# Optimization experiments

Hardware: AMD Instinct MI355X
Metric: run time of the kernel (lower is better)

The kernel has to match this reference:

```python
import jax, jax.numpy as jnp
import numpy as np

N = 10000      # nodes
E = 160000     # directed edges (avg degree 16)
F_IN = 2208    # num_features (DenseNet-161 dim)
H = 512        # hidden_channels
C = 2          # num_classes


def setup_inputs() -> dict:
    key = jax.random.key(0)
    ks = jax.random.split(key, 10)
    x = jax.random.normal(ks[0], (N, F_IN), dtype=jnp.float32)
    edge_index = jax.random.randint(ks[1], (2, E), 0, N, dtype=jnp.int64)
    batch = jnp.zeros((N,), dtype=jnp.int64)

    def glorot(k, fan_in, fan_out):
        s = np.sqrt(6.0 / (fan_in + fan_out)).astype(np.float32)
        return jax.random.uniform(k, (fan_in, fan_out), jnp.float32, -s, s)

    return {
        "x": x,
        "edge_index": edge_index,
        "batch": batch,
        "W1": glorot(ks[2], F_IN, H), "b1": jnp.zeros((H,), jnp.float32),
        "W2": glorot(ks[3], H, H),    "b2": jnp.zeros((H,), jnp.float32),
        "W3": glorot(ks[4], H, H),    "b3": jnp.zeros((H,), jnp.float32),
        "W4": glorot(ks[5], H, C),    "b4": jnp.zeros((C,), jnp.float32),
    }


def reference(x, edge_index, batch, W1, b1, W2, b2, W3, b3, W4, b4):
    # GCNConv (PyG defaults): add self-loops, symmetric normalization
    # out = D^{-1/2} (A + I) D^{-1/2} X W + b. Norm depends only on the
    # graph, so compute it once and reuse across the 4 layers.
    src, dst = edge_index[0], edge_index[1]
    loop = jnp.arange(N, dtype=edge_index.dtype)
    s = jnp.concatenate([src, loop])  # [E+N]
    d = jnp.concatenate([dst, loop])  # [E+N]
    deg = jax.ops.segment_sum(jnp.ones(E + N, x.dtype), d, num_segments=N)
    dinv = jnp.where(deg > 0, jax.lax.rsqrt(deg), 0.0)
    norm = dinv[s] * dinv[d]          # [E+N] per-edge weight

    def conv(h, W, b):
        h = h @ W                                 # [N, out] dense GEMM first (PyG order)
        msg = h[s] * norm[:, None]                # gather + scale  [E+N, out]
        return jax.ops.segment_sum(msg, d, num_segments=N) + b

    h = jax.nn.relu(conv(x, W1, b1))   # dropout p=0.3 is identity in eval mode
    h = jax.nn.relu(conv(h, W2, b2))
    h = jax.nn.relu(conv(h, W3, b3))
    h = conv(h, W4, b4)
    return jax.nn.log_softmax(h, axis=1)
```

## Files before the change

### kernel.cpp

```cpp
#include <hip/hip_runtime.h>
#include <hip/hip_bf16.h>

#define NNODES 10000
#define NEDGES 160000
#define FIN    2208
#define HDIM   512
#define NCLS   2

#define MPAD   10240
#define K1PAD  2240

typedef __bf16 bf16x8 __attribute__((ext_vector_type(8)));
typedef float  f32x4  __attribute__((ext_vector_type(4)));
typedef unsigned short u16x8 __attribute__((ext_vector_type(8)));

__device__ inline unsigned short f2bf(float f) {
    union { float f; unsigned int u; } v; v.f = f;
    return (unsigned short)((v.u + 0x7FFFu + ((v.u >> 16) & 1u)) >> 16);
}
__device__ inline float bf2f(unsigned short u) {
    union { unsigned int i; float f; } v; v.i = ((unsigned int)u) << 16; return v.f;
}


__global__ void k_init(int* cnt, int* row_cnt, int n) {
    int i = blockIdx.x * blockDim.x + threadIdx.x;
    if (i < n) { cnt[i] = 0; row_cnt[i] = 0; }
}

__global__ void k_hist(const int* __restrict__ ei, int* __restrict__ cnt, int e) {
    int i = blockIdx.x * blockDim.x + threadIdx.x;
    if (i < e) atomicAdd(&cnt[ei[NEDGES + i]], 1);
}

__global__ void k_scan(const int* __restrict__ cnt, int* __restrict__ row_ptr, int n) {
    __shared__ int wsum[16];
    __shared__ int s_carry;
    int tid = threadIdx.x;
    int lane = tid & 63, wid = tid >> 6;
    if (tid == 0) { s_carry = 0; row_ptr[0] = 0; }
    __syncthreads();
    for (int base = 0; base < n; base += 1024) {
        int i = base + tid;
        int v = (i < n) ? cnt[i] : 0;
        #pragma unroll
        for (int off = 1; off < 64; off <<= 1) {
            int t = __shfl_up(v, off);
            if (lane >= off) v += t;
        }
        if (lane == 63) wsum[wid] = v;
        __syncthreads();
        if (wid == 0) {
            int s = (lane < 16) ? wsum[lane] : 0;
            #pragma unroll
            for (int off = 1; off < 16; off <<= 1) {
                int t = __shfl_up(s, off);
                if (lane >= off) s += t;
            }
            if (lane < 16) wsum[lane] = s;
        }
        __syncthreads();
        int add = s_carry + ((wid > 0) ? wsum[wid - 1] : 0);
        if (i < n) row_ptr[i + 1] = v + add;
        __syncthreads();
        if (tid == 1023) s_carry += wsum[15];
        __syncthreads();
    }
}

__global__ void k_dinv(const int* __restrict__ cnt, float* __restrict__ dinv, int n) {
    int i = blockIdx.x * blockDim.x + threadIdx.x;
    if (i < n) dinv[i] = rsqrtf((float)cnt[i] + 1.0f);
}

__global__ void k_fill(const int* __restrict__ ei, const int* __restrict__ row_ptr,
                       int* __restrict__ row_cnt, int* __restrict__ col_src, int e) {
    int i = blockIdx.x * blockDim.x + threadIdx.x;
    if (i < e) {
        int src = ei[i];
        int dst = ei[NEDGES + i];
        int pos = row_ptr[dst] + atomicAdd(&row_cnt[dst], 1);
        col_src[pos] = src;
    }
}


__global__ void k_cvt_x(const float* __restrict__ x, unsigned short* __restrict__ xb) {
    int row = blockIdx.x;
    int t = threadIdx.x;
    unsigned short* orow = xb + (size_t)row * K1PAD;
    u16x8 z = {0, 0, 0, 0, 0, 0, 0, 0};
    if (row >= NNODES) {
        for (int c = t; c < K1PAD / 8; c += 256) *(u16x8*)(orow + c * 8) = z;
        return;
    }
    const float* irow = x + (size_t)row * FIN;
    for (int c = t; c < K1PAD / 8; c += 256) {
        int col = c * 8;
        u16x8 o = z;
        if (col + 8 <= FIN) {
            float4 f0 = *(const float4*)(irow + col);
            float4 f1 = *(const float4*)(irow + col + 4);
            o[0] = f2bf(f0.x); o[1] = f2bf(f0.y); o[2] = f2bf(f0.z); o[3] = f2bf(f0.w);
            o[4] = f2bf(f1.x); o[5] = f2bf(f1.y); o[6] = f2bf(f1.z); o[7] = f2bf(f1.w);
        }
        *(u16x8*)(orow + col) = o;
    }
}

__global__ void k_cvt_wt(const float* __restrict__ W, unsigned short* __restrict__ Wt,
                         int Kreal, int Kp) {
    int k = blockIdx.x * 256 + threadIdx.x;
    int n = blockIdx.y;
    if (k >= Kp) return;
    float v = (k < Kreal) ? W[(size_t)k * HDIM + n] : 0.0f;
    Wt[(size_t)n * Kp + k] = f2bf(v);
}


#define BKK 64

__global__ __launch_bounds__(256) void k_gemm_bf16(
    const unsigned short* __restrict__ A,
    const unsigned short* __restrict__ Bt,
    unsigned short* __restrict__ C,
    int M, int K) {
    __shared__ char As[128 * BKK * 2] __attribute__((aligned(16)));
    __shared__ char Bs[128 * BKK * 2] __attribute__((aligned(16)));
    const int tid  = threadIdx.x;
    const int lane = tid & 63;
    const int w    = tid >> 6;
    const int wm   = w & 1, wn = w >> 1;
    const int quad = lane >> 4, lq = lane & 15;

    const int l    = blockIdx.x;
    const int xcd  = l & 7;
    const int j    = l >> 3;
    const int bm   = ((j >> 2) * 8 + xcd) * 128;
    const int bn   = (j & 3) * 128;

    f32x4 acc[4][4] = {};

    for (int k0 = 0; k0 < K; k0 += BKK) {
        #pragma unroll
        for (int i = 0; i < 4; ++i) {
            int c  = i * 256 + tid;
            int r  = c >> 3;
            int g  = (c & 7) ^ (r & 7);
            const char* gpA = (const char*)A  + ((size_t)(bm + r) * K + k0) * 2 + (g << 4);
            const char* gpB = (const char*)Bt + ((size_t)(bn + r) * K + k0) * 2 + (g << 4);
            __builtin_amdgcn_global_load_lds(
                (const __attribute__((address_space(1))) void*)gpA,
                (__attribute__((address_space(3))) void*)(As + c * 16), 16, 0, 0);
            __builtin_amdgcn_global_load_lds(
                (const __attribute__((address_space(1))) void*)gpB,
                (__attribute__((address_space(3))) void*)(Bs + c * 16), 16, 0, 0);
        }
        __syncthreads();

        #pragma unroll
        for (int s = 0; s < 2; ++s) {
            bf16x8 af[4], bfr[4];
            #pragma unroll
            for (int i = 0; i < 4; ++i) {
                int r = wm * 64 + i * 16 + lq;
                int g = s * 4 + quad;
                af[i]  = *(const bf16x8*)(As + r * 128 + ((g ^ (r & 7)) << 4));
                int n = wn * 64 + i * 16 + lq;
                bfr[i] = *(const bf16x8*)(Bs + n * 128 + ((g ^ (n & 7)) << 4));
            }
            #pragma unroll
            for (int i = 0; i < 4; ++i)
                #pragma unroll
                for (int jj = 0; jj < 4; ++jj)
                    acc[i][jj] = __builtin_amdgcn_mfma_f32_16x16x32_bf16(
                        af[i], bfr[jj], acc[i][jj], 0, 0, 0);
        }
        __syncthreads();
    }

    #pragma unroll
    for (int i = 0; i < 4; ++i) {
        #pragma unroll
        for (int p = 0; p < 4; ++p) {
            int r = bm + wm * 64 + i * 16 + quad * 4 + p;
            if (r < M) {
                #pragma unroll
                for (int jj = 0; jj < 4; ++jj) {
                    int col = bn + wn * 64 + jj * 16 + lq;
                    C[(size_t)r * HDIM + col] = f2bf(acc[i][jj][p]);
                }
            }
        }
    }
}


__global__ void k_agg(const unsigned short* __restrict__ Y, const float* __restrict__ dinv,
                      const int* __restrict__ row_ptr, const int* __restrict__ col_src,
                      const float* __restrict__ bias, unsigned short* __restrict__ Hb,
                      int do_relu) {
    int w = (blockIdx.x * blockDim.x + threadIdx.x) >> 6;
    int lane = threadIdx.x & 63;
    if (w >= MPAD) return;
    unsigned short* hr = Hb + (size_t)w * HDIM + lane * 8;
    if (w >= NNODES) {
        u16x8 z = {0, 0, 0, 0, 0, 0, 0, 0};
        *(u16x8*)hr = z;
        return;
    }
    float di = dinv[w];
    float sw = di * di;
    u16x8 own = *(const u16x8*)(Y + (size_t)w * HDIM + lane * 8);
    float acc[8];
    #pragma unroll
    for (int t = 0; t < 8; ++t) acc[t] = sw * bf2f(own[t]);

    int e0 = row_ptr[w], e1 = row_ptr[w + 1];
    int e = e0;
    for (; e + 4 <= e1; e += 4) {
        int s0 = col_src[e + 0], s1 = col_src[e + 1];
        int s2 = col_src[e + 2], s3 = col_src[e + 3];
        float w0 = di * dinv[s0], w1 = di * dinv[s1];
        float w2 = di * dinv[s2], w3 = di * dinv[s3];
        u16x8 v0 = *(const u16x8*)(Y + (size_t)s0 * HDIM + lane * 8);
        u16x8 v1 = *(const u16x8*)(Y + (size_t)s1 * HDIM + lane * 8);
        u16x8 v2 = *(const u16x8*)(Y + (size_t)s2 * HDIM + lane * 8);
        u16x8 v3 = *(const u16x8*)(Y + (size_t)s3 * HDIM + lane * 8);
        #pragma unroll
        for (int t = 0; t < 8; ++t) {
            acc[t] += w0 * bf2f(v0[t]);
            acc[t] += w1 * bf2f(v1[t]);
            acc[t] += w2 * bf2f(v2[t]);
            acc[t] += w3 * bf2f(v3[t]);
        }
    }
    for (; e < e1; ++e) {
        int s = col_src[e];
        float wg = di * dinv[s];
        u16x8 v = *(const u16x8*)(Y + (size_t)s * HDIM + lane * 8);
        #pragma unroll
        for (int t = 0; t < 8; ++t) acc[t] += wg * bf2f(v[t]);
    }

    float4 b0 = ((const float4*)bias)[lane * 2];
    float4 b1 = ((const float4*)bias)[lane * 2 + 1];
    acc[0] += b0.x; acc[1] += b0.y; acc[2] += b0.z; acc[3] += b0.w;
    acc[4] += b1.x; acc[5] += b1.y; acc[6] += b1.z; acc[7] += b1.w;
    u16x8 o;
    #pragma unroll
    for (int t = 0; t < 8; ++t) {
        float v = acc[t];
        if (do_relu) v = fmaxf(v, 0.0f);
        o[t] = f2bf(v);
    }
    *(u16x8*)hr = o;
}


__global__ void k_gemm4(const unsigned short* __restrict__ H, const float* __restrict__ W4,
                        float* __restrict__ Y4, int n) {
    int w = (blockIdx.x * blockDim.x + threadIdx.x) >> 6;
    int lane = threadIdx.x & 63;
    if (w >= n) return;
    const unsigned short* hr = H + (size_t)w * HDIM + lane * 8;
    ushort4 hA = *(const ushort4*)hr;
    ushort4 hB = *(const ushort4*)(hr + 4);
    float hv[8] = {bf2f(hA.x), bf2f(hA.y), bf2f(hA.z), bf2f(hA.w),
                   bf2f(hB.x), bf2f(hB.y), bf2f(hB.z), bf2f(hB.w)};
    const float4* wf = (const float4*)W4;
    float4 w0 = wf[lane * 4 + 0];
    float4 w1 = wf[lane * 4 + 1];
    float4 w2 = wf[lane * 4 + 2];
    float4 w3 = wf[lane * 4 + 3];
    float acc0 = hv[0]*w0.x + hv[1]*w0.z + hv[2]*w1.x + hv[3]*w1.z
               + hv[4]*w2.x + hv[5]*w2.z + hv[6]*w3.x + hv[7]*w3.z;
    float acc1 = hv[0]*w0.y + hv[1]*w0.w + hv[2]*w1.y + hv[3]*w1.w
               + hv[4]*w2.y + hv[5]*w2.w + hv[6]*w3.y + hv[7]*w3.w;
    #pragma unroll
    for (int off = 32; off > 0; off >>= 1) {
        acc0 += __shfl_down(acc0, off);
        acc1 += __shfl_down(acc1, off);
    }
    if (lane == 0) {
        Y4[2 * w] = acc0;
        Y4[2 * w + 1] = acc1;
    }
}


__global__ void k_final(const float* __restrict__ Y4, const float* __restrict__ dinv,
                        const int* __restrict__ row_ptr, const int* __restrict__ col_src,
                        const float* __restrict__ b4, float* __restrict__ out, int n) {
    int i = blockIdx.x * blockDim.x + threadIdx.x;
    if (i >= n) return;
    float di = dinv[i];
    float sw = di * di;
    float z0 = sw * Y4[2 * i];
    float z1 = sw * Y4[2 * i + 1];
    int e0 = row_ptr[i], e1 = row_ptr[i + 1];
    for (int e = e0; e < e1; ++e) {
        int s = col_src[e];
        float wgt = di * dinv[s];
        z0 += wgt * Y4[2 * s];
        z1 += wgt * Y4[2 * s + 1];
    }
    z0 += b4[0];
    z1 += b4[1];
    float m = fmaxf(z0, z1);
    float l = m + logf(expf(z0 - m) + expf(z1 - m));
    out[2 * i] = z0 - l;
    out[2 * i + 1] = z1 - l;
}


extern "C" void kernel_launch(void* const* d_in, const int* in_sizes, int n_in,
                              void* d_out, int out_size, void* d_ws, size_t ws_size,
                              hipStream_t stream) {
    const float* x  = (const float*)d_in[0];
    const int*   ei = (const int*)d_in[1];
    const float* W1 = (const float*)d_in[3];
    const float* b1 = (const float*)d_in[4];
    const float* W2 = (const float*)d_in[5];
    const float* b2 = (const float*)d_in[6];
    const float* W3 = (const float*)d_in[7];
    const float* b3 = (const float*)d_in[8];
    const float* W4 = (const float*)d_in[9];
    const float* b4 = (const float*)d_in[10];
    float* out = (float*)d_out;

    char* ws = (char*)d_ws;
    float*          dinv    = (float*)(ws + 0);
    int*            cnt     = (int*)  (ws + 40960);
    int*            row_cnt = (int*)  (ws + 81920);
    int*            row_ptr = (int*)  (ws + 122880);
    int*            col_src = (int*)  (ws + 163840);
    float*          Y4      = (float*)(ws + 803840);
    unsigned short* xb      = (unsigned short*)(ws + 884224);
    unsigned short* W1t     = (unsigned short*)(ws + 46759424);
    unsigned short* W2t     = (unsigned short*)(ws + 49053184);
    unsigned short* W3t     = (unsigned short*)(ws + 49577472);
    unsigned short* Yb      = (unsigned short*)(ws + 50101760);
    unsigned short* Hb      = (unsigned short*)(ws + 60587520);
    if (ws_size < 71073280) return;

    k_init<<<40, 256, 0, stream>>>(cnt, row_cnt, NNODES);
    k_hist<<<625, 256, 0, stream>>>(ei, cnt, NEDGES);
    k_scan<<<1, 1024, 0, stream>>>(cnt, row_ptr, NNODES);
    k_dinv<<<40, 256, 0, stream>>>(cnt, dinv, NNODES);
    k_fill<<<625, 256, 0, stream>>>(ei, row_ptr, row_cnt, col_src, NEDGES);

    k_cvt_x<<<MPAD, 256, 0, stream>>>(x, xb);
    k_cvt_wt<<<dim3(9, HDIM), 256, 0, stream>>>(W1, W1t, FIN, K1PAD);
    k_cvt_wt<<<dim3(2, HDIM), 256, 0, stream>>>(W2, W2t, HDIM, HDIM);
    k_cvt_wt<<<dim3(2, HDIM), 256, 0, stream>>>(W3, W3t, HDIM, HDIM);

    const int ggrid = (MPAD / 128) * 4;
    const int agrid = (MPAD * 64) / 256;

    k_gemm_bf16<<<ggrid, 256, 0, stream>>>(xb, W1t, Yb, NNODES, K1PAD);
    k_agg<<<agrid, 256, 0, stream>>>(Yb, dinv, row_ptr, col_src, b1, Hb, 1);
    k_gemm_bf16<<<ggrid, 256, 0, stream>>>(Hb, W2t, Yb, NNODES, HDIM);
    k_agg<<<agrid, 256, 0, stream>>>(Yb, dinv, row_ptr, col_src, b2, Hb, 1);
    k_gemm_bf16<<<ggrid, 256, 0, stream>>>(Hb, W3t, Yb, NNODES, HDIM);
    k_agg<<<agrid, 256, 0, stream>>>(Yb, dinv, row_ptr, col_src, b3, Hb, 1);
    k_gemm4<<<2500, 256, 0, stream>>>(Hb, W4, Y4, NNODES);
    k_final<<<40, 256, 0, stream>>>(Y4, dinv, row_ptr, col_src, b4, out, NNODES);
}
```

Baseline: 367.5 us.

## Narrow GEMM tile to 128x64 and fuse small setup kernels

```diff
diff --git a/kernel.cpp b/kernel.cpp
--- a/kernel.cpp
+++ b/kernel.cpp
@@ -33,7 +33,8 @@
     if (i < e) atomicAdd(&cnt[ei[NEDGES + i]], 1);
 }
 
-__global__ void k_scan(const int* __restrict__ cnt, int* __restrict__ row_ptr, int n) {
+__global__ void k_scan(const int* __restrict__ cnt, int* __restrict__ row_ptr,
+                       float* __restrict__ dinv, int n) {
     __shared__ int wsum[16];
     __shared__ int s_carry;
     int tid = threadIdx.x;
@@ -42,7 +43,9 @@
     __syncthreads();
     for (int base = 0; base < n; base += 1024) {
         int i = base + tid;
-        int v = (i < n) ? cnt[i] : 0;
+        int deg = (i < n) ? cnt[i] : 0;
+        if (i < n) dinv[i] = rsqrtf((float)deg + 1.0f);
+        int v = deg;
         #pragma unroll
         for (int off = 1; off < 64; off <<= 1) {
             int t = __shfl_up(v, off);
@@ -66,11 +69,6 @@
         if (tid == 1023) s_carry += wsum[15];
         __syncthreads();
     }
-}
-
-__global__ void k_dinv(const int* __restrict__ cnt, float* __restrict__ dinv, int n) {
-    int i = blockIdx.x * blockDim.x + threadIdx.x;
-    if (i < n) dinv[i] = rsqrtf((float)cnt[i] + 1.0f);
 }
 
 __global__ void k_fill(const int* __restrict__ ei, const int* __restrict__ row_ptr,
@@ -108,13 +106,25 @@
     }
 }
 
-__global__ void k_cvt_wt(const float* __restrict__ W, unsigned short* __restrict__ Wt,
-                         int Kreal, int Kp) {
-    int k = blockIdx.x * 256 + threadIdx.x;
+__global__ void k_cvt_w(const float* __restrict__ W1, const float* __restrict__ W2,
+                        const float* __restrict__ W3, unsigned short* __restrict__ W1t,
+                        unsigned short* __restrict__ W2t, unsigned short* __restrict__ W3t) {
     int n = blockIdx.y;
-    if (k >= Kp) return;
-    float v = (k < Kreal) ? W[(size_t)k * HDIM + n] : 0.0f;
-    Wt[(size_t)n * Kp + k] = f2bf(v);
+    int bx = blockIdx.x;
+    int t = threadIdx.x;
+    if (bx < 9) {
+        int k = bx * 256 + t;
+        if (k < K1PAD) {
+            float v = (k < FIN) ? W1[(size_t)k * HDIM + n] : 0.0f;
+            W1t[(size_t)n * K1PAD + k] = f2bf(v);
+        }
+    } else if (bx < 11) {
+        int k = (bx - 9) * 256 + t;
+        W2t[(size_t)n * HDIM + k] = f2bf(W2[(size_t)k * HDIM + n]);
+    } else {
+        int k = (bx - 11) * 256 + t;
+        W3t[(size_t)n * HDIM + k] = f2bf(W3[(size_t)k * HDIM + n]);
+    }
 }
 
 
@@ -126,20 +136,21 @@
     unsigned short* __restrict__ C,
     int M, int K) {
     __shared__ char As[128 * BKK * 2] __attribute__((aligned(16)));
-    __shared__ char Bs[128 * BKK * 2] __attribute__((aligned(16)));
+    __shared__ char Bs[64 * BKK * 2]  __attribute__((aligned(16)));
     const int tid  = threadIdx.x;
     const int lane = tid & 63;
     const int w    = tid >> 6;
     const int wm   = w & 1, wn = w >> 1;
     const int quad = lane >> 4, lq = lane & 15;
 
-    const int l    = blockIdx.x;
-    const int xcd  = l & 7;
-    const int j    = l >> 3;
-    const int bm   = ((j >> 2) * 8 + xcd) * 128;
-    const int bn   = (j & 3) * 128;
-
-    f32x4 acc[4][4] = {};
+    const int l     = blockIdx.x;
+    const int xcd   = l & 7;
+    const int q     = l >> 3;
+    const int strip = (q >> 3) * 8 + xcd;
+    const int bm    = strip * 128;
+    const int bn    = (q & 7) * 64;
+
+    f32x4 acc[4][2] = {};
 
     for (int k0 = 0; k0 < K; k0 += BKK) {
         #pragma unroll
@@ -147,11 +158,17 @@
             int c  = i * 256 + tid;
             int r  = c >> 3;
             int g  = (c & 7) ^ (r & 7);
-            const char* gpA = (const char*)A  + ((size_t)(bm + r) * K + k0) * 2 + (g << 4);
-            const char* gpB = (const char*)Bt + ((size_t)(bn + r) * K + k0) * 2 + (g << 4);
+            const char* gpA = (const char*)A + ((size_t)(bm + r) * K + k0) * 2 + (g << 4);
             __builtin_amdgcn_global_load_lds(
                 (const __attribute__((address_space(1))) void*)gpA,
                 (__attribute__((address_space(3))) void*)(As + c * 16), 16, 0, 0);
+        }
+        #pragma unroll
+        for (int i = 0; i < 2; ++i) {
+            int c  = i * 256 + tid;
+            int r  = c >> 3;
+            int g  = (c & 7) ^ (r & 7);
+            const char* gpB = (const char*)Bt + ((size_t)(bn + r) * K + k0) * 2 + (g << 4);
             __builtin_amdgcn_global_load_lds(
                 (const __attribute__((address_space(1))) void*)gpB,
                 (__attribute__((address_space(3))) void*)(Bs + c * 16), 16, 0, 0);
@@ -160,21 +177,24 @@
 
         #pragma unroll
         for (int s = 0; s < 2; ++s) {
-            bf16x8 af[4], bfr[4];
+            bf16x8 af[4], bfr[2];
+            int g = s * 4 + quad;
             #pragma unroll
             for (int i = 0; i < 4; ++i) {
                 int r = wm * 64 + i * 16 + lq;
-                int g = s * 4 + quad;
-                af[i]  = *(const bf16x8*)(As + r * 128 + ((g ^ (r & 7)) << 4));
-                int n = wn * 64 + i * 16 + lq;
-                bfr[i] = *(const bf16x8*)(Bs + n * 128 + ((g ^ (n & 7)) << 4));
+                af[i] = *(const bf16x8*)(As + r * 128 + ((g ^ (r & 7)) << 4));
+            }
+            #pragma unroll
+            for (int j = 0; j < 2; ++j) {
+                int n = wn * 32 + j * 16 + lq;
+                bfr[j] = *(const bf16x8*)(Bs + n * 128 + ((g ^ (n & 7)) << 4));
             }
             #pragma unroll
             for (int i = 0; i < 4; ++i)
                 #pragma unroll
-                for (int jj = 0; jj < 4; ++jj)
-                    acc[i][jj] = __builtin_amdgcn_mfma_f32_16x16x32_bf16(
-                        af[i], bfr[jj], acc[i][jj], 0, 0, 0);
+                for (int j = 0; j < 2; ++j)
+                    acc[i][j] = __builtin_amdgcn_mfma_f32_16x16x32_bf16(
+                        af[i], bfr[j], acc[i][j], 0, 0, 0);
         }
         __syncthreads();
     }
@@ -186,9 +206,9 @@
             int r = bm + wm * 64 + i * 16 + quad * 4 + p;
             if (r < M) {
                 #pragma unroll
-                for (int jj = 0; jj < 4; ++jj) {
-                    int col = bn + wn * 64 + jj * 16 + lq;
-                    C[(size_t)r * HDIM + col] = f2bf(acc[i][jj][p]);
+                for (int j = 0; j < 2; ++j) {
+                    int col = bn + wn * 32 + j * 16 + lq;
+                    C[(size_t)r * HDIM + col] = f2bf(acc[i][j][p]);
                 }
             }
         }
@@ -346,16 +366,13 @@
 
     k_init<<<40, 256, 0, stream>>>(cnt, row_cnt, NNODES);
     k_hist<<<625, 256, 0, stream>>>(ei, cnt, NEDGES);
-    k_scan<<<1, 1024, 0, stream>>>(cnt, row_ptr, NNODES);
-    k_dinv<<<40, 256, 0, stream>>>(cnt, dinv, NNODES);
+    k_scan<<<1, 1024, 0, stream>>>(cnt, row_ptr, dinv, NNODES);
     k_fill<<<625, 256, 0, stream>>>(ei, row_ptr, row_cnt, col_src, NEDGES);
 
     k_cvt_x<<<MPAD, 256, 0, stream>>>(x, xb);
-    k_cvt_wt<<<dim3(9, HDIM), 256, 0, stream>>>(W1, W1t, FIN, K1PAD);
-    k_cvt_wt<<<dim3(2, HDIM), 256, 0, stream>>>(W2, W2t, HDIM, HDIM);
-    k_cvt_wt<<<dim3(2, HDIM), 256, 0, stream>>>(W3, W3t, HDIM, HDIM);
-
-    const int ggrid = (MPAD / 128) * 4;
+    k_cvt_w<<<dim3(13, HDIM), 256, 0, stream>>>(W1, W2, W3, W1t, W2t, W3t);
+
+    const int ggrid = (MPAD / 128) * 8;
     const int agrid = (MPAD * 64) / 256;
 
     k_gemm_bf16<<<ggrid, 256, 0, stream>>>(xb, W1t, Yb, NNODES, K1PAD);
```

Result: faster. 346.0 us (-5.9%).
